# Optimization experiments

Measured on AMD Instinct MI355X. Metric: run time of the kernel, lower is better.

The kernel has to match this reference:

```python
import jax, jax.numpy as jnp
import numpy as np

NUM_CLASSES = 2
TIME_STEPS = 1000
B = 16
L = 1024


def _cosine_schedule(num_steps, s=0.01):
    # Faithful port of beta_schedule(..., 'cosine') + __init__ log buffers (float64 -> float32).
    t = np.arange(0, num_steps + 1, dtype=np.float64)
    f_t = np.cos((t / num_steps + s) / (1 + s) * np.pi * 0.5) ** 2
    alpha_bars = f_t / f_t[0]
    alphas = np.clip(alpha_bars[1:] / alpha_bars[:-1], 0.001, 0.999)
    alphas = np.sqrt(alphas)
    log_alphas = np.log(alphas)
    log_alpha_bars = np.cumsum(log_alphas)
    log_1_minus_alphas = np.log(1.0 - np.exp(log_alphas) + 1e-40)
    log_1_minus_alpha_bars = np.log(1.0 - np.exp(log_alpha_bars) + 1e-40)
    f32 = lambda x: jnp.asarray(x, jnp.float32)
    return f32(log_alphas), f32(log_1_minus_alphas), f32(log_alpha_bars), f32(log_1_minus_alpha_bars)


def setup_inputs() -> dict:
    key = jax.random.key(0)
    k1, k2, k3 = jax.random.split(key, 3)
    # log_x_t: log one-hot, as produced by log_sample_categorical (clamp min 1e-30 -> log)
    x_t = jax.random.randint(k1, (B, 1, L, L), 0, NUM_CLASSES)
    onehot = jax.nn.one_hot(x_t, NUM_CLASSES, axis=1, dtype=jnp.float32)  # (B,K,1,L,L)
    log_x_t = jnp.log(jnp.clip(onehot, 1e-30))
    # log_x_0: log-softmax distribution, as produced by predict_x_0 (F.log_softmax over class dim)
    logits0 = jax.random.normal(k2, (B, NUM_CLASSES, 1, L, L), jnp.float32)
    log_x_0 = jax.nn.log_softmax(logits0, axis=1)
    la, l1a, lab, l1ab = _cosine_schedule(TIME_STEPS)
    t = jax.random.randint(k3, (B,), 0, TIME_STEPS).astype(jnp.int64)
    return {
        'log_x_t': log_x_t,
        'log_x_0': log_x_0,
        'log_alphas': la,
        'log_1_minus_alphas': l1a,
        'log_alpha_bars': lab,
        'log_1_minus_alpha_bars': l1ab,
        't': t,
    }


def reference(log_x_t, log_x_0, log_alphas, log_1_minus_alphas, log_alpha_bars, log_1_minus_alpha_bars, t):
    # MultinomialDiffusion.q_posterior: gather(extract) + log_add_exp + where-mask + logsumexp over class dim.
    K = log_x_0.shape[1]
    log_K = jnp.log(jnp.asarray(K, log_x_0.dtype))
    ext = lambda a, tt: a[tt].reshape(-1, 1, 1, 1, 1)  # extract(a, t, x_shape)

    # q_pred(log_x_0, t-1) with t-1 clamped to 0
    t_m1 = jnp.maximum(t - 1, 0)
    log_EV_qxtmin_x0 = jnp.logaddexp(
        log_x_0 + ext(log_alpha_bars, t_m1),
        ext(log_1_minus_alpha_bars, t_m1) - log_K,
    )
    # where t == 0, posterior mean is log_x_0 itself
    t_b = t.reshape(-1, 1, 1, 1, 1)
    log_EV_qxtmin_x0 = jnp.where(t_b == 0, log_x_0, log_EV_qxtmin_x0)

    # q_pred_one_step(log_x_t, t)
    log_one_step = jnp.logaddexp(
        log_x_t + ext(log_alphas, t),
        ext(log_1_minus_alphas, t) - log_K,
    )

    unnormed = log_EV_qxtmin_x0 + log_one_step
    return unnormed - jax.nn.logsumexp(unnormed, axis=1, keepdims=True)
```

## Files before the change

### kernel.cpp

```cpp
#include <hip/hip_runtime.h>


#define LL (1024 * 1024)
#define GROUPS_PER_PLANE (1 << 18)
#define NBLOCKS 2048
#define NTHREADS 256
#define GSTRIDE (NBLOCKS * NTHREADS)
#define NITER ((16 * GROUPS_PER_PLANE) / GSTRIDE)

typedef float vfloat4 __attribute__((ext_vector_type(4)));

__global__ __launch_bounds__(256) void qposterior_kernel(
    const float* __restrict__ lxt,
    const float* __restrict__ lx0,
    const float* __restrict__ la,
    const float* __restrict__ l1a,
    const float* __restrict__ lab,
    const float* __restrict__ l1ab,
    const int* __restrict__ tarr,
    float* __restrict__ out)
{
    const float LOGK = 0.6931471805599453f;

    int g = blockIdx.x * NTHREADS + threadIdx.x;

#pragma unroll 2
    for (int it = 0; it < NITER; ++it, g += GSTRIDE) {
        int b  = g >> 18;
        int eg = (g & (GROUPS_PER_PLANE - 1)) << 2;

        const float* xt_p  = lxt + b * (2 * LL) + eg;
        const float* x0_p  = lx0 + b * (2 * LL) + eg;
        float*       out_p = out + b * (2 * LL) + eg;

        vfloat4 xt4 = *reinterpret_cast<const vfloat4*>(xt_p);
        vfloat4 x04 = *reinterpret_cast<const vfloat4*>(x0_p);

        int tb = tarr[b];
        float C = la[tb];
        float D = l1a[tb] - LOGK;
        float mm = fmaxf(C, D);
        float s_hot = mm + __logf(1.0f + __expf(fminf(C, D) - mm));
        float delta = s_hot - D;

        vfloat4 r0, r1;
        if (tb != 0) {
            int tm1 = tb - 1;
            float a   = __expf(lab[tm1]);
            float c   = 0.5f * __expf(l1ab[tm1]);
            float apc = a + c;
            float Fp  = __expf(delta);
            float Fm  = __expf(-delta);
#pragma unroll
            for (int i = 0; i < 4; ++i) {
                float p  = __expf(x04[i]);
                float u  = fmaf(a, p, c);
                float v  = fmaf(-a, p, apc);
                bool hot = (xt4[i] > -35.0f);
                float F  = hot ? Fp : Fm;
                float sd = hot ? delta : -delta;
                float w  = fmaf(u, F, v);
                float lu = __logf(u);
                float lv = __logf(v);
                float lw = __logf(w);
                r0[i] = (lu - lw) + sd;
                r1[i] = lv - lw;
            }
        } else {
            vfloat4 x14 = *reinterpret_cast<const vfloat4*>(x0_p + LL);
#pragma unroll
            for (int i = 0; i < 4; ++i) {
                float d     = x04[i] - x14[i];
                float sd    = (xt4[i] > -35.0f) ? delta : -delta;
                float Delta = d + sd;
                float m  = fmaxf(-Delta, 0.0f);
                float o0 = -(m + __logf(1.0f + __expf(-fabsf(Delta))));
                r0[i] = o0;
                r1[i] = o0 - Delta;
            }
        }

        *reinterpret_cast<vfloat4*>(out_p)      = r0;
        *reinterpret_cast<vfloat4*>(out_p + LL) = r1;
    }
}

extern "C" void kernel_launch(void* const* d_in, const int* in_sizes, int n_in,
                              void* d_out, int out_size, void* d_ws, size_t ws_size,
                              hipStream_t stream) {
    const float* lxt  = (const float*)d_in[0];
    const float* lx0  = (const float*)d_in[1];
    const float* la   = (const float*)d_in[2];
    const float* l1a  = (const float*)d_in[3];
    const float* lab  = (const float*)d_in[4];
    const float* l1ab = (const float*)d_in[5];
    const int*   tarr = (const int*)d_in[6];
    float*       out  = (float*)d_out;

    qposterior_kernel<<<NBLOCKS, NTHREADS, 0, stream>>>(lxt, lx0, la, l1a, lab, l1ab, tarr, out);
}
```

Baseline: 293.6 us.

## Split into mask-precompute kernel and posterior kernel reading compact byte mask

```diff
diff --git a/kernel.cpp b/kernel.cpp
--- a/kernel.cpp
+++ b/kernel.cpp
@@ -2,15 +2,137 @@
 
 
 #define LL (1024 * 1024)
+#define BPB 512
+#define NBLK (16 * BPB)
+#define MASK_BYTES (NBLK * 256)
+
+typedef float vfloat4 __attribute__((ext_vector_type(4)));
+
+__device__ __forceinline__ int mask_idx(int bid, int tid) { return (bid << 8) | tid; }
+
+__global__ __launch_bounds__(256) void mask_kernel(
+    const float* __restrict__ lxt, unsigned char* __restrict__ mask)
+{
+    int bid   = blockIdx.x;
+    int b     = bid >> 9;
+    int local = bid & (BPB - 1);
+    int e0    = local * 2048 + threadIdx.x * 4;
+
+    const float* xt_p = lxt + b * (2 * LL);
+    vfloat4 xa = *reinterpret_cast<const vfloat4*>(xt_p + e0);
+    vfloat4 xb = *reinterpret_cast<const vfloat4*>(xt_p + e0 + 1024);
+
+    unsigned int m = 0;
+#pragma unroll
+    for (int j = 0; j < 4; ++j) m |= (xa[j] > -35.0f ? 1u : 0u) << j;
+#pragma unroll
+    for (int j = 0; j < 4; ++j) m |= (xb[j] > -35.0f ? 1u : 0u) << (4 + j);
+
+    mask[mask_idx(bid, threadIdx.x)] = (unsigned char)m;
+}
+
+__global__ __launch_bounds__(256) void qpost_kernel(
+    const float* __restrict__ lx0,
+    const unsigned char* __restrict__ mask,
+    const float* __restrict__ la,
+    const float* __restrict__ l1a,
+    const float* __restrict__ lab,
+    const float* __restrict__ l1ab,
+    const int* __restrict__ tarr,
+    float* __restrict__ out)
+{
+    const float LOGK = 0.6931471805599453f;
+
+    int bid   = blockIdx.x;
+    int b     = bid >> 9;
+    int local = bid & (BPB - 1);
+    int e0    = local * 2048 + threadIdx.x * 4;
+
+    const float* x0_p  = lx0 + b * (2 * LL);
+    float*       out_p = out + b * (2 * LL);
+
+    vfloat4 A  = *reinterpret_cast<const vfloat4*>(x0_p + e0);
+    vfloat4 Bv = *reinterpret_cast<const vfloat4*>(x0_p + e0 + 1024);
+    unsigned int m = mask[mask_idx(bid, threadIdx.x)];
+
+    int tb = tarr[b];
+    float C = la[tb];
+    float D = l1a[tb] - LOGK;
+    float mm = fmaxf(C, D);
+    float s_hot = mm + __logf(1.0f + __expf(fminf(C, D) - mm));
+    float delta = s_hot - D;
+
+    vfloat4 r0a, r1a, r0b, r1b;
+    if (tb != 0) {
+        int tm1 = tb - 1;
+        float a   = __expf(lab[tm1]);
+        float c   = 0.5f * __expf(l1ab[tm1]);
+        float apc = a + c;
+        float Fp  = __expf(delta);
+        float Fm  = __expf(-delta);
+#pragma unroll
+        for (int i = 0; i < 4; ++i) {
+            float p  = __expf(A[i]);
+            float u  = fmaf(a, p, c);
+            float v  = fmaf(-a, p, apc);
+            bool hot = (m >> i) & 1u;
+            float F  = hot ? Fp : Fm;
+            float sd = hot ? delta : -delta;
+            float w  = fmaf(u, F, v);
+            float lw = __logf(w);
+            r0a[i] = (__logf(u) - lw) + sd;
+            r1a[i] = __logf(v) - lw;
+        }
+#pragma unroll
+        for (int i = 0; i < 4; ++i) {
+            float p  = __expf(Bv[i]);
+            float u  = fmaf(a, p, c);
+            float v  = fmaf(-a, p, apc);
+            bool hot = (m >> (4 + i)) & 1u;
+            float F  = hot ? Fp : Fm;
+            float sd = hot ? delta : -delta;
+            float w  = fmaf(u, F, v);
+            float lw = __logf(w);
+            r0b[i] = (__logf(u) - lw) + sd;
+            r1b[i] = __logf(v) - lw;
+        }
+    } else {
+        vfloat4 x1a = *reinterpret_cast<const vfloat4*>(x0_p + e0 + LL);
+        vfloat4 x1b = *reinterpret_cast<const vfloat4*>(x0_p + e0 + 1024 + LL);
+#pragma unroll
+        for (int i = 0; i < 4; ++i) {
+            float d     = A[i] - x1a[i];
+            float sd    = ((m >> i) & 1u) ? delta : -delta;
+            float Delta = d + sd;
+            float mo = fmaxf(-Delta, 0.0f);
+            float o0 = -(mo + __logf(1.0f + __expf(-fabsf(Delta))));
+            r0a[i] = o0;
+            r1a[i] = o0 - Delta;
+        }
+#pragma unroll
+        for (int i = 0; i < 4; ++i) {
+            float d     = Bv[i] - x1b[i];
+            float sd    = ((m >> (4 + i)) & 1u) ? delta : -delta;
+            float Delta = d + sd;
+            float mo = fmaxf(-Delta, 0.0f);
+            float o0 = -(mo + __logf(1.0f + __expf(-fabsf(Delta))));
+            r0b[i] = o0;
+            r1b[i] = o0 - Delta;
+        }
+    }
+
+    *reinterpret_cast<vfloat4*>(out_p + e0)              = r0a;
+    *reinterpret_cast<vfloat4*>(out_p + e0 + 1024)       = r0b;
+    *reinterpret_cast<vfloat4*>(out_p + e0 + LL)         = r1a;
+    *reinterpret_cast<vfloat4*>(out_p + e0 + 1024 + LL)  = r1b;
+}
+
 #define GROUPS_PER_PLANE (1 << 18)
-#define NBLOCKS 2048
-#define NTHREADS 256
-#define GSTRIDE (NBLOCKS * NTHREADS)
-#define NITER ((16 * GROUPS_PER_PLANE) / GSTRIDE)
-
-typedef float vfloat4 __attribute__((ext_vector_type(4)));
-
-__global__ __launch_bounds__(256) void qposterior_kernel(
+#define FB_NBLOCKS 2048
+#define FB_GSTRIDE (FB_NBLOCKS * 256)
+#define FB_NITER ((16 * GROUPS_PER_PLANE) / FB_GSTRIDE)
+
+__global__ __launch_bounds__(256) void qposterior_fused(
     const float* __restrict__ lxt,
     const float* __restrict__ lx0,
     const float* __restrict__ la,
@@ -21,28 +143,22 @@
     float* __restrict__ out)
 {
     const float LOGK = 0.6931471805599453f;
-
-    int g = blockIdx.x * NTHREADS + threadIdx.x;
-
+    int g = blockIdx.x * 256 + threadIdx.x;
 #pragma unroll 2
-    for (int it = 0; it < NITER; ++it, g += GSTRIDE) {
+    for (int it = 0; it < FB_NITER; ++it, g += FB_GSTRIDE) {
         int b  = g >> 18;
         int eg = (g & (GROUPS_PER_PLANE - 1)) << 2;
-
         const float* xt_p  = lxt + b * (2 * LL) + eg;
         const float* x0_p  = lx0 + b * (2 * LL) + eg;
         float*       out_p = out + b * (2 * LL) + eg;
-
         vfloat4 xt4 = *reinterpret_cast<const vfloat4*>(xt_p);
         vfloat4 x04 = *reinterpret_cast<const vfloat4*>(x0_p);
-
         int tb = tarr[b];
         float C = la[tb];
         float D = l1a[tb] - LOGK;
         float mm = fmaxf(C, D);
         float s_hot = mm + __logf(1.0f + __expf(fminf(C, D) - mm));
         float delta = s_hot - D;
-
         vfloat4 r0, r1;
         if (tb != 0) {
             int tm1 = tb - 1;
@@ -60,11 +176,9 @@
                 float F  = hot ? Fp : Fm;
                 float sd = hot ? delta : -delta;
                 float w  = fmaf(u, F, v);
-                float lu = __logf(u);
-                float lv = __logf(v);
                 float lw = __logf(w);
-                r0[i] = (lu - lw) + sd;
-                r1[i] = lv - lw;
+                r0[i] = (__logf(u) - lw) + sd;
+                r1[i] = __logf(v) - lw;
             }
         } else {
             vfloat4 x14 = *reinterpret_cast<const vfloat4*>(x0_p + LL);
@@ -73,13 +187,12 @@
                 float d     = x04[i] - x14[i];
                 float sd    = (xt4[i] > -35.0f) ? delta : -delta;
                 float Delta = d + sd;
-                float m  = fmaxf(-Delta, 0.0f);
-                float o0 = -(m + __logf(1.0f + __expf(-fabsf(Delta))));
+                float mo = fmaxf(-Delta, 0.0f);
+                float o0 = -(mo + __logf(1.0f + __expf(-fabsf(Delta))));
                 r0[i] = o0;
                 r1[i] = o0 - Delta;
             }
         }
-
         *reinterpret_cast<vfloat4*>(out_p)      = r0;
         *reinterpret_cast<vfloat4*>(out_p + LL) = r1;
     }
@@ -97,5 +210,11 @@
     const int*   tarr = (const int*)d_in[6];
     float*       out  = (float*)d_out;
 
-    qposterior_kernel<<<NBLOCKS, NTHREADS, 0, stream>>>(lxt, lx0, la, l1a, lab, l1ab, tarr, out);
-}
+    if (d_ws != nullptr && ws_size >= (size_t)MASK_BYTES) {
+        unsigned char* mask = (unsigned char*)d_ws;
+        mask_kernel<<<NBLK, 256, 0, stream>>>(lxt, mask);
+        qpost_kernel<<<NBLK, 256, 0, stream>>>(lx0, mask, la, l1a, lab, l1ab, tarr, out);
+    } else {
+        qposterior_fused<<<FB_NBLOCKS, 256, 0, stream>>>(lxt, lx0, la, l1a, lab, l1ab, tarr, out);
+    }
+}
```

New measurement: 289.0 us. Within noise of the previous version (-1.5%).
